# Performance work log

Measured on AMD Instinct MI355X. Metric: run time of the kernel, lower is better.

Reference implementation:

```python
import jax, jax.numpy as jnp
import numpy as np

B, S, HIDDEN = 2, 2048, 2048
HQ, HKV, D = 16, 4, 128
EPS = 1e-6
SCALE = D ** -0.5


def _deinterleave(x):
    # [..., D] interleaved pairs -> [x0,x2,...,x1,x3,...] (half layout)
    *lead, d = x.shape
    return x.reshape(*lead, d // 2, 2).swapaxes(-1, -2).reshape(*lead, d)


def _interleave(x):
    # inverse of _deinterleave
    *lead, d = x.shape
    return x.reshape(*lead, 2, d // 2).swapaxes(-1, -2).reshape(*lead, d)


def _rotate_half(x):
    x1, x2 = jnp.split(x, 2, axis=-1)
    return jnp.concatenate([-x2, x1], axis=-1)


def _rmsnorm(x, w):
    var = jnp.mean(jnp.square(x), axis=-1, keepdims=True)
    return x * jax.lax.rsqrt(var + EPS) * w


def setup_inputs() -> dict:
    key = jax.random.key(0)
    k0, k1, k2, k3, k4 = jax.random.split(key, 5)
    hidden_states = jax.random.normal(k0, (B, S, HIDDEN), jnp.float32)
    cos = jax.random.uniform(k1, (S, D), jnp.float32, -1.0, 1.0)
    sin = jax.random.uniform(k2, (S, D), jnp.float32, -1.0, 1.0)
    qkv_w = jax.random.normal(k3, ((HQ + 2 * HKV) * D, HIDDEN), jnp.float32) * 0.02
    qk_norm_w = jnp.ones((D,), jnp.float32)
    o_w = jax.random.normal(k4, (HIDDEN, HQ * D), jnp.float32) * 0.02
    return {"hidden_states": hidden_states, "cos": cos, "sin": sin,
            "qkv_w": qkv_w, "qk_norm_w": qk_norm_w, "o_w": o_w}


def reference(hidden_states, cos, sin, qkv_w, qk_norm_w, o_w):
    b, s, _ = hidden_states.shape
    qkv = jnp.einsum('bsh,oh->bso', hidden_states, qkv_w)  # [B,S,(HQ+2HKV)*D]
    q = qkv[..., : HQ * D].reshape(b, s, HQ, D)
    k = qkv[..., HQ * D:(HQ + HKV) * D].reshape(b, s, HKV, D)
    v = qkv[..., (HQ + HKV) * D:].reshape(b, s, HKV, D)

    # interleaved-layout RoPE: deinterleave -> rotate-half RoPE -> re-interleave
    q, k = _deinterleave(q), _deinterleave(k)
    cs = cos[None, :, None, :]
    sn = sin[None, :, None, :]
    q = q * cs + _rotate_half(q) * sn
    k = k * cs + _rotate_half(k) * sn
    q, k = _interleave(q), _interleave(k)

    # QK RMSNorm (shared weight over head_dim)
    q = _rmsnorm(q, qk_norm_w)
    k = _rmsnorm(k, qk_norm_w)

    # causal GQA attention
    g = HQ // HKV
    qg = q.reshape(b, s, HKV, g, D)
    scores = jnp.einsum('bshgd,bthd->bhgst', qg, k) * SCALE  # [B,HKV,g,S,S]
    causal = jnp.tril(jnp.ones((s, s), bool))
    scores = jnp.where(causal, scores, jnp.finfo(scores.dtype).min)
    probs = jax.nn.softmax(scores, axis=-1)
    attn = jnp.einsum('bhgst,bthd->bshgd', probs, v).reshape(b, s, HQ * D)

    return jnp.einsum('bsd,od->bso', attn, o_w)
```

## Files before the change

### kernel.cpp

```cpp
#include <hip/hip_runtime.h>
#include <hip/hip_bf16.h>

typedef __bf16 bf16_t;
typedef bf16_t bf16x8 __attribute__((ext_vector_type(8)));
typedef float f32x4 __attribute__((ext_vector_type(4)));
typedef float f32x16 __attribute__((ext_vector_type(16)));
typedef unsigned short u16;
typedef unsigned int u32;

#define B_    2
#define S_    2048
#define HID   2048
#define NQKV  3072
#define HQ_   16
#define HKV_  4
#define D_    128
#define QSCALE_ 0.12751879526600565f

__device__ __forceinline__ u16 f2b(float f) {
    __hip_bfloat16 h = __float2bfloat16(f);
    return *reinterpret_cast<u16*>(&h);
}

__global__ __launch_bounds__(256) void cvt_f32_bf16(const float* __restrict__ in,
                                                    u16* __restrict__ out, int n4) {
    int i = blockIdx.x * 256 + threadIdx.x;
    if (i >= n4) return;
    float4 v = reinterpret_cast<const float4*>(in)[i];
    ushort4 o;
    o.x = f2b(v.x); o.y = f2b(v.y); o.z = f2b(v.z); o.w = f2b(v.w);
    reinterpret_cast<ushort4*>(out)[i] = o;
}

__global__ __launch_bounds__(512, 1) void gemm256_bt(const u16* __restrict__ A,
                                                     const u16* __restrict__ Bm,
                                                     float* __restrict__ C,
                                                     int M, int N, int K) {
    extern __shared__ __align__(16) char smem[];
    u16* Asm = (u16*)smem;
    u16* Bsm = (u16*)smem + 32768;

    const int tid  = threadIdx.x;
    const int lane = tid & 63;
    const int wid  = tid >> 6;
    const int wr = wid >> 2, wc = wid & 3;
    const int lrow = lane & 15, lgrp = lane >> 4;
    const int swz  = (lrow & 7) << 4;
    const int m0 = blockIdx.x * 256, n0 = blockIdx.y * 256;

    const int stRow = tid >> 3;
    const int stCol = ((((tid & 7) * 16) ^ ((stRow & 7) << 4)) >> 1);

    const u16* aBase = A  + (size_t)(m0 + stRow) * K + stCol;
    const u16* bBase = Bm + (size_t)(n0 + stRow) * K + stCol;

    auto glds = [&](const u16* g, u16* l) {
        __builtin_amdgcn_global_load_lds(
            (const __attribute__((address_space(1))) void*)g,
            (__attribute__((address_space(3))) void*)l, 16, 0, 0);
    };
    auto stageA = [&](int buf, int h, int k0) {
        const u16* g = aBase + (size_t)(128 * h) * K + k0;
        u16* d = Asm + buf * 16384 + (1024 * h + tid) * 8;
        glds(g, d);
        glds(g + (size_t)64 * K, d + 512 * 8);
    };
    auto stageB = [&](int buf, int h, int k0) {
        const u16* g = bBase + (size_t)(128 * h) * K + k0;
        u16* d = Bsm + buf * 16384 + (1024 * h + tid) * 8;
        glds(g, d);
        glds(g + (size_t)64 * K, d + 512 * 8);
    };

    f32x4 acc[8][4] = {};
    const int KT = K >> 6;

    stageA(0, 0, 0); stageA(0, 1, 0); stageB(0, 0, 0); stageB(0, 1, 0);
    asm volatile("s_waitcnt vmcnt(0)" ::: "memory");
    __builtin_amdgcn_s_barrier();

    for (int x = 0; x < KT; ++x) {
        const int cur = x & 1;
        const int kn  = (x + 1) << 6;
        const bool pf = (x + 1 < KT);
        const char* aT = (const char*)(Asm + cur * 16384);
        const char* bT = (const char*)(Bsm + cur * 16384);

        auto ldA = [&](int mi, int ks) -> bf16x8 {
            int row = wr * 128 + mi * 16 + lrow;
            return *(const bf16x8*)(aT + row * 128 + ((ks * 64 + lgrp * 16) ^ swz));
        };
        auto ldB = [&](int ni, int ks) -> bf16x8 {
            int row = wc * 64 + ni * 16 + lrow;
            return *(const bf16x8*)(bT + row * 128 + ((ks * 64 + lgrp * 16) ^ swz));
        };

        bf16x8 a[4][2], b[2][2], b2[2][2];

        #pragma unroll
        for (int mi = 0; mi < 4; ++mi) { a[mi][0] = ldA(mi, 0); a[mi][1] = ldA(mi, 1); }
        #pragma unroll
        for (int ni = 0; ni < 2; ++ni) { b[ni][0] = ldB(ni, 0); b[ni][1] = ldB(ni, 1); }
        if (pf) stageA(cur ^ 1, 0, kn);
        __builtin_amdgcn_s_barrier();
        __builtin_amdgcn_s_setprio(1);
        #pragma unroll
        for (int mi = 0; mi < 4; ++mi)
            #pragma unroll
            for (int ni = 0; ni < 2; ++ni) {
                acc[mi][ni] = __builtin_amdgcn_mfma_f32_16x16x32_bf16(a[mi][0], b[ni][0], acc[mi][ni], 0, 0, 0);
                acc[mi][ni] = __builtin_amdgcn_mfma_f32_16x16x32_bf16(a[mi][1], b[ni][1], acc[mi][ni], 0, 0, 0);
            }
        __builtin_amdgcn_s_setprio(0);
        __builtin_amdgcn_s_barrier();

        #pragma unroll
        for (int ni = 0; ni < 2; ++ni) { b2[ni][0] = ldB(ni + 2, 0); b2[ni][1] = ldB(ni + 2, 1); }
        if (pf) stageA(cur ^ 1, 1, kn);
        __builtin_amdgcn_s_barrier();
        __builtin_amdgcn_s_setprio(1);
        #pragma unroll
        for (int mi = 0; mi < 4; ++mi)
            #pragma unroll
            for (int ni = 0; ni < 2; ++ni) {
                acc[mi][ni + 2] = __builtin_amdgcn_mfma_f32_16x16x32_bf16(a[mi][0], b2[ni][0], acc[mi][ni + 2], 0, 0, 0);
                acc[mi][ni + 2] = __builtin_amdgcn_mfma_f32_16x16x32_bf16(a[mi][1], b2[ni][1], acc[mi][ni + 2], 0, 0, 0);
            }
        __builtin_amdgcn_s_setprio(0);
        __builtin_amdgcn_s_barrier();

        #pragma unroll
        for (int mi = 0; mi < 4; ++mi) { a[mi][0] = ldA(mi + 4, 0); a[mi][1] = ldA(mi + 4, 1); }
        if (pf) stageB(cur ^ 1, 0, kn);
        __builtin_amdgcn_s_barrier();
        __builtin_amdgcn_s_setprio(1);
        #pragma unroll
        for (int mi = 0; mi < 4; ++mi)
            #pragma unroll
            for (int ni = 0; ni < 2; ++ni) {
                acc[mi + 4][ni + 2] = __builtin_amdgcn_mfma_f32_16x16x32_bf16(a[mi][0], b2[ni][0], acc[mi + 4][ni + 2], 0, 0, 0);
                acc[mi + 4][ni + 2] = __builtin_amdgcn_mfma_f32_16x16x32_bf16(a[mi][1], b2[ni][1], acc[mi + 4][ni + 2], 0, 0, 0);
            }
        __builtin_amdgcn_s_setprio(0);
        __builtin_amdgcn_s_barrier();

        #pragma unroll
        for (int ni = 0; ni < 2; ++ni) { b[ni][0] = ldB(ni, 0); b[ni][1] = ldB(ni, 1); }
        if (pf) stageB(cur ^ 1, 1, kn);
        __builtin_amdgcn_s_barrier();
        __builtin_amdgcn_s_setprio(1);
        #pragma unroll
        for (int mi = 0; mi < 4; ++mi)
            #pragma unroll
            for (int ni = 0; ni < 2; ++ni) {
                acc[mi + 4][ni] = __builtin_amdgcn_mfma_f32_16x16x32_bf16(a[mi][0], b[ni][0], acc[mi + 4][ni], 0, 0, 0);
                acc[mi + 4][ni] = __builtin_amdgcn_mfma_f32_16x16x32_bf16(a[mi][1], b[ni][1], acc[mi + 4][ni], 0, 0, 0);
            }
        __builtin_amdgcn_s_setprio(0);
        asm volatile("s_waitcnt vmcnt(0)" ::: "memory");
        __builtin_amdgcn_s_barrier();
    }

    #pragma unroll
    for (int mi = 0; mi < 8; ++mi)
        #pragma unroll
        for (int ni = 0; ni < 4; ++ni) {
            int r = m0 + wr * 128 + mi * 16 + lgrp * 4;
            int c = n0 + wc * 64 + ni * 16 + lrow;
            float* p = C + (size_t)r * N + c;
            #pragma unroll
            for (int i = 0; i < 4; ++i) p[(size_t)i * N] = acc[mi][ni][i];
        }
}

__global__ __launch_bounds__(256) void rope_norm_split(const float* __restrict__ qkv,
                                                       const float* __restrict__ cosb,
                                                       const float* __restrict__ sinb,
                                                       const float* __restrict__ nw,
                                                       u16* __restrict__ qb,
                                                       u16* __restrict__ kb,
                                                       u16* __restrict__ vb) {
    const int row  = blockIdx.x;
    const int b    = row >> 11;
    const int s    = row & 2047;
    const int wave = threadIdx.x >> 6;
    const int lane = threadIdx.x & 63;
    const float* base = qkv + (size_t)row * NQKV;

    const float c0 = cosb[s * 128 + lane];
    const float c1 = cosb[s * 128 + 64 + lane];
    const float s0 = sinb[s * 128 + lane];
    const float s1 = sinb[s * 128 + 64 + lane];
    const float w0 = nw[2 * lane];
    const float w1 = nw[2 * lane + 1];

    for (int h = wave; h < HQ_ + HKV_; h += 4) {
        float2 x = *(const float2*)(base + h * 128 + 2 * lane);
        float y0 = x.x * c0 - x.y * s0;
        float y1 = x.y * c1 + x.x * s1;
        float ss = y0 * y0 + y1 * y1;
        #pragma unroll
        for (int off = 32; off; off >>= 1) ss += __shfl_xor(ss, off);
        float r = rsqrtf(ss * (1.0f / 128.0f) + 1e-6f);
        float o0 = y0 * r * w0, o1 = y1 * r * w1;
        if (h < HQ_) {
            u32 pack = (u32)f2b(o0 * QSCALE_) | ((u32)f2b(o1 * QSCALE_) << 16);
            *(u32*)(qb + ((size_t)(b * HQ_ + h) * S_ + s) * D_ + 2 * lane) = pack;
        } else {
            u32 pack = (u32)f2b(o0) | ((u32)f2b(o1) << 16);
            *(u32*)(kb + ((size_t)(b * HKV_ + (h - HQ_)) * S_ + s) * D_ + 2 * lane) = pack;
        }
    }
    {
        int h = wave;
        float2 x = *(const float2*)(base + (HQ_ + HKV_) * 128 + h * 128 + 2 * lane);
        u32 pack = (u32)f2b(x.x) | ((u32)f2b(x.y) << 16);
        *(u32*)(vb + ((size_t)(b * HKV_ + h) * S_ + s) * D_ + 2 * lane) = pack;
    }
}

__global__ __launch_bounds__(256) void transpose_v(const u16* __restrict__ vb,
                                                   u16* __restrict__ vtb) {
    __shared__ u16 t[64][72];
    const int s0 = blockIdx.x * 64, d0 = blockIdx.y * 64, bh = blockIdx.z;
    const u16* src = vb  + (size_t)bh * S_ * D_;
    u16*       dst = vtb + (size_t)bh * D_ * S_;
    const int tid = threadIdx.x;

    {
        int r = tid >> 3, c8 = (tid & 7) * 8;
        #pragma unroll
        for (int p = 0; p < 2; p++) {
            int rr = r + p * 32;
            *(uint4*)&t[rr][c8] = *(const uint4*)(src + (size_t)(s0 + rr) * D_ + d0 + c8);
        }
    }
    __syncthreads();
    {
        int dd = tid & 63;
        int sb = (tid >> 6) * 8;
        #pragma unroll
        for (int p = 0; p < 2; p++) {
            int ss8 = sb + p * 32;
            union { u16 u[8]; uint4 v; } pk;
            #pragma unroll
            for (int j = 0; j < 8; j++) pk.u[j] = t[ss8 + j][dd];
            *(uint4*)(dst + (size_t)(d0 + dd) * S_ + s0 + ss8) = pk.v;
        }
    }
}

__global__ __launch_bounds__(256, 2) void attn_fwd3(const u16* __restrict__ qb,
                                                    const u16* __restrict__ kb,
                                                    const u16* __restrict__ vtb,
                                                    u16* __restrict__ attn) {
    __shared__ __align__(16) u16 Ks[2][64 * 128];
    __shared__ __align__(16) u16 Vs[2][128 * 64];

    const int bh  = blockIdx.y;
    const int qt  = (bh < 16) ? (15 - (int)blockIdx.x) : (int)blockIdx.x;
    const int b   = bh >> 4, hq = bh & 15, hkv = hq >> 2;
    const int tid = threadIdx.x;
    const int wave = tid >> 6, lane = tid & 63;
    const int l31 = lane & 31, hi = lane >> 5;
    const int swz = (l31 & 7) << 4;

    const u16* Q  = qb  + (size_t)(b * HQ_  + hq ) * S_ * D_;
    const u16* Kp = kb  + (size_t)(b * HKV_ + hkv) * S_ * D_;
    const u16* Vt = vtb + (size_t)(b * HKV_ + hkv) * D_ * S_;
    const int q0w = qt * 128 + wave * 32;
    const int qg  = q0w + l31;

    int kSrc[4], vSrc[4], cLds[4];
    #pragma unroll
    for (int p = 0; p < 4; p++) {
        int c = tid + p * 256;
        int kr = c >> 4, kc = ((c & 15) * 16) ^ ((kr & 7) << 4);
        kSrc[p] = kr * D_ + (kc >> 1);
        int vr = c >> 3, vc = ((c & 7) * 16) ^ ((vr & 7) << 4);
        vSrc[p] = vr * S_ + (vc >> 1);
        cLds[p] = c * 16;
    }

    auto STAGE = [&](int buf, int kv0s) {
        const u16* kbase = Kp + (size_t)kv0s * D_;
        const u16* vbase = Vt + kv0s;
        #pragma unroll
        for (int p = 0; p < 4; p++)
            __builtin_amdgcn_global_load_lds(
                (const __attribute__((address_space(1))) void*)(kbase + kSrc[p]),
                (__attribute__((address_space(3))) void*)((char*)Ks[buf] + cLds[p]), 16, 0, 0);
        #pragma unroll
        for (int p = 0; p < 4; p++)
            __builtin_amdgcn_global_load_lds(
                (const __attribute__((address_space(1))) void*)(vbase + vSrc[p]),
                (__attribute__((address_space(3))) void*)((char*)Vs[buf] + cLds[p]), 16, 0, 0);
    };

    bf16x8 qf[8];
    #pragma unroll
    for (int ds = 0; ds < 8; ds++)
        qf[ds] = *(const bf16x8*)(Q + (size_t)qg * D_ + ds * 16 + hi * 8);

    float m_run = -1e30f, l_run = 0.f;
    f32x16 oacc[4] = {};

    const int nkt = 2 * qt + 2;
    STAGE(0, 0);

    for (int kt = 0; kt < nkt; kt++) {
        const int cur = kt & 1;
        const int kv0 = kt * 64;
        if (kt + 1 < nkt) {
            STAGE(cur ^ 1, kv0 + 64);
            asm volatile("s_waitcnt vmcnt(8)" ::: "memory");
        } else {
            asm volatile("s_waitcnt vmcnt(0)" ::: "memory");
        }
        __builtin_amdgcn_s_barrier();

        const char* ksb = (const char*)Ks[cur];
        const char* vsb = (const char*)Vs[cur];
        const char* rb0 = ksb + l31 * 256;
        const char* rb1 = rb0 + 32 * 256;
        bf16x8 kA[8], kB[8];
        #pragma unroll
        for (int ds = 0; ds < 8; ds++) kA[ds] = *(const bf16x8*)(rb0 + ((ds * 32 + hi * 16) ^ swz));
        #pragma unroll
        for (int ds = 0; ds < 8; ds++) kB[ds] = *(const bf16x8*)(rb1 + ((ds * 32 + hi * 16) ^ swz));

        f32x16 sc[2] = {};
        __builtin_amdgcn_s_setprio(1);
        #pragma unroll
        for (int ds = 0; ds < 8; ds++)
            sc[0] = __builtin_amdgcn_mfma_f32_32x32x16_bf16(kA[ds], qf[ds], sc[0], 0, 0, 0);
        #pragma unroll
        for (int ds = 0; ds < 8; ds++)
            sc[1] = __builtin_amdgcn_mfma_f32_32x32x16_bf16(kB[ds], qf[ds], sc[1], 0, 0, 0);
        __builtin_amdgcn_s_setprio(0);

        bf16x8 vf[4][4];
        #pragma unroll
        for (int ks = 0; ks < 4; ks++)
            #pragma unroll
            for (int d4 = 0; d4 < 4; d4++)
                vf[ks][d4] = *(const bf16x8*)(vsb + (d4 * 32 + l31) * 128
                                                  + ((ks * 32 + hi * 16) ^ swz));
        __builtin_amdgcn_s_barrier();

        if (kv0 + 63 > q0w) {
            #pragma unroll
            for (int blk = 0; blk < 2; blk++)
                #pragma unroll
                for (int r = 0; r < 16; r++) {
                    int kvg = kv0 + blk * 32 + (r & 3) + 8 * (r >> 2) + 4 * hi;
                    if (kvg > qg) sc[blk][r] = -1e30f;
                }
        }

        float t16[16];
        #pragma unroll
        for (int r = 0; r < 16; r++) t16[r] = fmaxf(sc[0][r], sc[1][r]);
        #pragma unroll
        for (int r = 0; r < 8; r++) t16[r] = fmaxf(t16[r], t16[r + 8]);
        #pragma unroll
        for (int r = 0; r < 4; r++) t16[r] = fmaxf(t16[r], t16[r + 4]);
        float mt = fmaxf(fmaxf(t16[0], t16[1]), fmaxf(t16[2], t16[3]));
        mt = fmaxf(mt, __shfl_xor(mt, 32));

        bool noDefer = !__all(mt <= m_run + 8.0f);
        float mnew = m_run;
        if (noDefer) {
            mnew = fmaxf(m_run, mt);
            float alpha = __builtin_amdgcn_exp2f(m_run - mnew);
            l_run *= alpha;
            #pragma unroll
            for (int d4 = 0; d4 < 4; d4++)
                #pragma unroll
                for (int r = 0; r < 16; r++) oacc[d4][r] *= alpha;
            m_run = mnew;
        }

        float la = 0.f;
        u32 pk0[8], pk1[8];
        #pragma unroll
        for (int g = 0; g < 4; g++)
            #pragma unroll
            for (int e = 0; e < 2; e++) {
                float a0 = __builtin_amdgcn_exp2f(sc[0][g * 4 + 2 * e]     - mnew);
                float b0 = __builtin_amdgcn_exp2f(sc[0][g * 4 + 2 * e + 1] - mnew);
                float a1 = __builtin_amdgcn_exp2f(sc[1][g * 4 + 2 * e]     - mnew);
                float b1 = __builtin_amdgcn_exp2f(sc[1][g * 4 + 2 * e + 1] - mnew);
                la += (a0 + b0) + (a1 + b1);
                pk0[g * 2 + e] = (u32)f2b(a0) | ((u32)f2b(b0) << 16);
                pk1[g * 2 + e] = (u32)f2b(a1) | ((u32)f2b(b1) << 16);
            }
        la += __shfl_xor(la, 32);
        l_run += la;

        u32 qk0[8], qk1[8];
        #pragma unroll
        for (int i = 0; i < 8; i++) {
            qk0[i] = __shfl_xor(pk0[i], 32);
            qk1[i] = __shfl_xor(pk1[i], 32);
        }

        #pragma unroll
        for (int ks = 0; ks < 4; ks++) {
            const int i0 = (ks & 1) * 4;
            union { u32 w[4]; bf16x8 v; } pfv;
            if (ks & 2) {
                pfv.w[0] = hi ? qk1[i0 + 2] : pk1[i0 + 0];
                pfv.w[1] = hi ? qk1[i0 + 3] : pk1[i0 + 1];
                pfv.w[2] = hi ? pk1[i0 + 2] : qk1[i0 + 0];
                pfv.w[3] = hi ? pk1[i0 + 3] : qk1[i0 + 1];
            } else {
                pfv.w[0] = hi ? qk0[i0 + 2] : pk0[i0 + 0];
                pfv.w[1] = hi ? qk0[i0 + 3] : pk0[i0 + 1];
                pfv.w[2] = hi ? pk0[i0 + 2] : qk0[i0 + 0];
                pfv.w[3] = hi ? pk0[i0 + 3] : qk0[i0 + 1];
            }
            __builtin_amdgcn_s_setprio(1);
            #pragma unroll
            for (int d4 = 0; d4 < 4; d4++)
                oacc[d4] = __builtin_amdgcn_mfma_f32_32x32x16_bf16(vf[ks][d4], pfv.v, oacc[d4], 0, 0, 0);
            __builtin_amdgcn_s_setprio(0);
        }
    }

    const float inv = 1.0f / l_run;
    u16* sl = (u16*)Ks + wave * (32 * 128);
    #pragma unroll
    for (int d4 = 0; d4 < 4; d4++)
        #pragma unroll
        for (int rp = 0; rp < 8; rp++) {
            int dbyte = d4 * 64 + 16 * (rp >> 1) + 8 * hi + 4 * (rp & 1);
            u32 w = (u32)f2b(oacc[d4][rp * 2] * inv)
                  | ((u32)f2b(oacc[d4][rp * 2 + 1] * inv) << 16);
            *(u32*)((char*)sl + l31 * 256 + (dbyte ^ swz)) = w;
        }
    #pragma unroll
    for (int j = 0; j < 8; j++) {
        int c = lane + j * 64;
        int qL = c >> 4, dc = c & 15;
        uint4 v = *(uint4*)((char*)sl + qL * 256 + ((dc * 16) ^ ((qL & 7) << 4)));
        int qrow = qt * 128 + wave * 32 + qL;
        *(uint4*)(attn + (size_t)(b * S_ + qrow) * (HQ_ * D_) + hq * D_ + dc * 8) = v;
    }
}

extern "C" void kernel_launch(void* const* d_in, const int* in_sizes, int n_in,
                              void* d_out, int out_size, void* d_ws, size_t ws_size,
                              hipStream_t stream) {
    const float* hidden = (const float*)d_in[0];
    const float* cosb   = (const float*)d_in[1];
    const float* sinb   = (const float*)d_in[2];
    const float* qkvw   = (const float*)d_in[3];
    const float* nw     = (const float*)d_in[4];
    const float* ow     = (const float*)d_in[5];
    float* out = (float*)d_out;

    const size_t M  = (size_t)B_ * S_;
    char* ws = (char*)d_ws;
    size_t off = 0;
    u16*   hb    = (u16*)(ws + off); off += M * HID * 2;
    u16*   wqkvb = (u16*)(ws + off); off += (size_t)NQKV * HID * 2;
    u16*   wob   = (u16*)(ws + off); off += (size_t)HID * (HQ_ * D_) * 2;
    float* qkv   = (float*)(ws + off); off += M * NQKV * 4;
    u16*   qb2   = (u16*)(ws + off); off += (size_t)B_ * HQ_  * S_ * D_ * 2;
    u16*   kb2   = (u16*)(ws + off); off += (size_t)B_ * HKV_ * S_ * D_ * 2;
    u16*   vb2   = (u16*)(ws + off); off += (size_t)B_ * HKV_ * S_ * D_ * 2;
    u16*   vtb   = (u16*)(ws + off); off += (size_t)B_ * HKV_ * S_ * D_ * 2;
    u16*   attn  = hb;

    {
        int n4 = (int)(M * HID / 4);
        cvt_f32_bf16<<<(n4 + 255) / 256, 256, 0, stream>>>(hidden, hb, n4);
    }
    {
        int n4 = NQKV * HID / 4;
        cvt_f32_bf16<<<(n4 + 255) / 256, 256, 0, stream>>>(qkvw, wqkvb, n4);
    }
    {
        int n4 = HID * (HQ_ * D_) / 4;
        cvt_f32_bf16<<<(n4 + 255) / 256, 256, 0, stream>>>(ow, wob, n4);
    }

    const int smemSz = 131072;
    hipFuncSetAttribute(reinterpret_cast<const void*>(gemm256_bt),
                        hipFuncAttributeMaxDynamicSharedMemorySize, smemSz);

    gemm256_bt<<<dim3(M / 256, NQKV / 256), 512, smemSz, stream>>>(hb, wqkvb, qkv,
                                                                   (int)M, NQKV, HID);

    rope_norm_split<<<(int)M, 256, 0, stream>>>(qkv, cosb, sinb, nw, qb2, kb2, vb2);

    transpose_v<<<dim3(S_ / 64, D_ / 64, B_ * HKV_), 256, 0, stream>>>(vb2, vtb);

    attn_fwd3<<<dim3(16, B_ * HQ_), 256, 0, stream>>>(qb2, kb2, vtb, attn);

    gemm256_bt<<<dim3(M / 256, HID / 256), 512, smemSz, stream>>>(attn, wob, out,
                                                                  (int)M, HID, HQ_ * D_);
}
```

Baseline: 234.2 us.

## Shrink GEMM tiles to 128x256, emit bf16 QKV, single-buffer V in attention

The GEMM tile goes from 256x256 to 128x256, which doubles the block count so the CUs are better filled, and adds an XCD-aware block swizzle. The whole next K-tile is now prefetched up front and there are fewer barriers. The QKV GEMM now writes bf16 directly, which halves intermediate traffic, and rope_norm reads bf16. The attention kernel single-buffers V to raise occupancy to 3 blocks and reorders the grid so heads vary fastest. The risks are lower per-block reuse in the GEMM, V loads that are exposed, and slightly lower precision because qkv is rounded before RoPE and norm.

```diff
diff --git a/kernel.cpp b/kernel.cpp
--- a/kernel.cpp
+++ b/kernel.cpp
@@ -21,6 +21,12 @@
     __hip_bfloat16 h = __float2bfloat16(f);
     return *reinterpret_cast<u16*>(&h);
 }
+__device__ __forceinline__ float b2f(u32 u) {
+    u32 v = u << 16;
+    float f;
+    __builtin_memcpy(&f, &v, 4);
+    return f;
+}
 
 __global__ __launch_bounds__(256) void cvt_f32_bf16(const float* __restrict__ in,
                                                     u16* __restrict__ out, int n4) {
@@ -32,13 +38,12 @@
     reinterpret_cast<ushort4*>(out)[i] = o;
 }
 
-__global__ __launch_bounds__(512, 1) void gemm256_bt(const u16* __restrict__ A,
-                                                     const u16* __restrict__ Bm,
-                                                     float* __restrict__ C,
-                                                     int M, int N, int K) {
+template<bool BF16OUT>
+__global__ __launch_bounds__(512, 1) void gemm128x256(const u16* __restrict__ A,
+                                                      const u16* __restrict__ Bm,
+                                                      void* __restrict__ Cv,
+                                                      int M, int N, int K) {
     extern __shared__ __align__(16) char smem[];
-    u16* Asm = (u16*)smem;
-    u16* Bsm = (u16*)smem + 32768;
 
     const int tid  = threadIdx.x;
     const int lane = tid & 63;
@@ -46,11 +51,15 @@
     const int wr = wid >> 2, wc = wid & 3;
     const int lrow = lane & 15, lgrp = lane >> 4;
     const int swz  = (lrow & 7) << 4;
-    const int m0 = blockIdx.x * 256, n0 = blockIdx.y * 256;
+
+    const int gx = gridDim.x;
+    const int nwg = gx * gridDim.y;
+    const int id = blockIdx.x + blockIdx.y * gx;
+    const int swid = (id & 7) * (nwg >> 3) + (id >> 3);
+    const int m0 = (swid % gx) * 128, n0 = (swid / gx) * 256;
 
     const int stRow = tid >> 3;
     const int stCol = ((((tid & 7) * 16) ^ ((stRow & 7) << 4)) >> 1);
-
     const u16* aBase = A  + (size_t)(m0 + stRow) * K + stCol;
     const u16* bBase = Bm + (size_t)(n0 + stRow) * K + stCol;
 
@@ -59,35 +68,34 @@
             (const __attribute__((address_space(1))) void*)g,
             (__attribute__((address_space(3))) void*)l, 16, 0, 0);
     };
-    auto stageA = [&](int buf, int h, int k0) {
-        const u16* g = aBase + (size_t)(128 * h) * K + k0;
-        u16* d = Asm + buf * 16384 + (1024 * h + tid) * 8;
+    auto stA = [&](int buf, int k0) {
+        u16* d = (u16*)(smem + buf * 49152) + tid * 8;
+        glds(aBase + k0, d);
+        glds(aBase + (size_t)64 * K + k0, d + 512 * 8);
+    };
+    auto stB = [&](int buf, int h, int k0) {
+        u16* d = (u16*)(smem + buf * 49152 + 16384 + h * 16384) + tid * 8;
+        const u16* g = bBase + (size_t)(128 * h) * K + k0;
         glds(g, d);
         glds(g + (size_t)64 * K, d + 512 * 8);
     };
-    auto stageB = [&](int buf, int h, int k0) {
-        const u16* g = bBase + (size_t)(128 * h) * K + k0;
-        u16* d = Bsm + buf * 16384 + (1024 * h + tid) * 8;
-        glds(g, d);
-        glds(g + (size_t)64 * K, d + 512 * 8);
-    };
-
-    f32x4 acc[8][4] = {};
+
+    f32x4 acc[4][4] = {};
     const int KT = K >> 6;
 
-    stageA(0, 0, 0); stageA(0, 1, 0); stageB(0, 0, 0); stageB(0, 1, 0);
+    stA(0, 0); stB(0, 0, 0); stB(0, 1, 0);
     asm volatile("s_waitcnt vmcnt(0)" ::: "memory");
     __builtin_amdgcn_s_barrier();
 
-    for (int x = 0; x < KT; ++x) {
-        const int cur = x & 1;
-        const int kn  = (x + 1) << 6;
-        const bool pf = (x + 1 < KT);
-        const char* aT = (const char*)(Asm + cur * 16384);
-        const char* bT = (const char*)(Bsm + cur * 16384);
+    for (int t = 0; t < KT; ++t) {
+        const int cur = t & 1;
+        const int kn  = (t + 1) << 6;
+        const bool pf = (t + 1 < KT);
+        const char* aT = smem + cur * 49152;
+        const char* bT = aT + 16384;
 
         auto ldA = [&](int mi, int ks) -> bf16x8 {
-            int row = wr * 128 + mi * 16 + lrow;
+            int row = wr * 64 + mi * 16 + lrow;
             return *(const bf16x8*)(aT + row * 128 + ((ks * 64 + lgrp * 16) ^ swz));
         };
         auto ldB = [&](int ni, int ks) -> bf16x8 {
@@ -101,7 +109,7 @@
         for (int mi = 0; mi < 4; ++mi) { a[mi][0] = ldA(mi, 0); a[mi][1] = ldA(mi, 1); }
         #pragma unroll
         for (int ni = 0; ni < 2; ++ni) { b[ni][0] = ldB(ni, 0); b[ni][1] = ldB(ni, 1); }
-        if (pf) stageA(cur ^ 1, 0, kn);
+        if (pf) { stA(cur ^ 1, kn); stB(cur ^ 1, 0, kn); stB(cur ^ 1, 1, kn); }
         __builtin_amdgcn_s_barrier();
         __builtin_amdgcn_s_setprio(1);
         #pragma unroll
@@ -112,11 +120,9 @@
                 acc[mi][ni] = __builtin_amdgcn_mfma_f32_16x16x32_bf16(a[mi][1], b[ni][1], acc[mi][ni], 0, 0, 0);
             }
         __builtin_amdgcn_s_setprio(0);
-        __builtin_amdgcn_s_barrier();
 
         #pragma unroll
         for (int ni = 0; ni < 2; ++ni) { b2[ni][0] = ldB(ni + 2, 0); b2[ni][1] = ldB(ni + 2, 1); }
-        if (pf) stageA(cur ^ 1, 1, kn);
         __builtin_amdgcn_s_barrier();
         __builtin_amdgcn_s_setprio(1);
         #pragma unroll
@@ -127,53 +133,31 @@
                 acc[mi][ni + 2] = __builtin_amdgcn_mfma_f32_16x16x32_bf16(a[mi][1], b2[ni][1], acc[mi][ni + 2], 0, 0, 0);
             }
         __builtin_amdgcn_s_setprio(0);
-        __builtin_amdgcn_s_barrier();
-
-        #pragma unroll
-        for (int mi = 0; mi < 4; ++mi) { a[mi][0] = ldA(mi + 4, 0); a[mi][1] = ldA(mi + 4, 1); }
-        if (pf) stageB(cur ^ 1, 0, kn);
-        __builtin_amdgcn_s_barrier();
-        __builtin_amdgcn_s_setprio(1);
-        #pragma unroll
-        for (int mi = 0; mi < 4; ++mi)
-            #pragma unroll
-            for (int ni = 0; ni < 2; ++ni) {
-                acc[mi + 4][ni + 2] = __builtin_amdgcn_mfma_f32_16x16x32_bf16(a[mi][0], b2[ni][0], acc[mi + 4][ni + 2], 0, 0, 0);
-                acc[mi + 4][ni + 2] = __builtin_amdgcn_mfma_f32_16x16x32_bf16(a[mi][1], b2[ni][1], acc[mi + 4][ni + 2], 0, 0, 0);
+        if (pf) {
+            asm volatile("s_waitcnt vmcnt(0)" ::: "memory");
+            __builtin_amdgcn_s_barrier();
+        }
+    }
+
+    #pragma unroll
+    for (int mi = 0; mi < 4; ++mi)
+        #pragma unroll
+        for (int ni = 0; ni < 4; ++ni) {
+            int r = m0 + wr * 64 + mi * 16 + lgrp * 4;
+            int c = n0 + wc * 64 + ni * 16 + lrow;
+            if (BF16OUT) {
+                u16* o = (u16*)Cv + (size_t)r * N + c;
+                #pragma unroll
+                for (int i = 0; i < 4; ++i) o[(size_t)i * N] = f2b(acc[mi][ni][i]);
+            } else {
+                float* p = (float*)Cv + (size_t)r * N + c;
+                #pragma unroll
+                for (int i = 0; i < 4; ++i) p[(size_t)i * N] = acc[mi][ni][i];
             }
-        __builtin_amdgcn_s_setprio(0);
-        __builtin_amdgcn_s_barrier();
-
-        #pragma unroll
-        for (int ni = 0; ni < 2; ++ni) { b[ni][0] = ldB(ni, 0); b[ni][1] = ldB(ni, 1); }
-        if (pf) stageB(cur ^ 1, 1, kn);
-        __builtin_amdgcn_s_barrier();
-        __builtin_amdgcn_s_setprio(1);
-        #pragma unroll
-        for (int mi = 0; mi < 4; ++mi)
-            #pragma unroll
-            for (int ni = 0; ni < 2; ++ni) {
-                acc[mi + 4][ni] = __builtin_amdgcn_mfma_f32_16x16x32_bf16(a[mi][0], b[ni][0], acc[mi + 4][ni], 0, 0, 0);
-                acc[mi + 4][ni] = __builtin_amdgcn_mfma_f32_16x16x32_bf16(a[mi][1], b[ni][1], acc[mi + 4][ni], 0, 0, 0);
-            }
-        __builtin_amdgcn_s_setprio(0);
-        asm volatile("s_waitcnt vmcnt(0)" ::: "memory");
-        __builtin_amdgcn_s_barrier();
-    }
-
-    #pragma unroll
-    for (int mi = 0; mi < 8; ++mi)
-        #pragma unroll
-        for (int ni = 0; ni < 4; ++ni) {
-            int r = m0 + wr * 128 + mi * 16 + lgrp * 4;
-            int c = n0 + wc * 64 + ni * 16 + lrow;
-            float* p = C + (size_t)r * N + c;
-            #pragma unroll
-            for (int i = 0; i < 4; ++i) p[(size_t)i * N] = acc[mi][ni][i];
-        }
-}
-
-__global__ __launch_bounds__(256) void rope_norm_split(const float* __restrict__ qkv,
+        }
+}
+
+__global__ __launch_bounds__(256) void rope_norm_split(const u16* __restrict__ qkvb,
                                                        const float* __restrict__ cosb,
                                                        const float* __restrict__ sinb,
                                                        const float* __restrict__ nw,
@@ -185,7 +169,7 @@
     const int s    = row & 2047;
     const int wave = threadIdx.x >> 6;
     const int lane = threadIdx.x & 63;
-    const float* base = qkv + (size_t)row * NQKV;
+    const u16* base = qkvb + (size_t)row * NQKV;
 
     const float c0 = cosb[s * 128 + lane];
     const float c1 = cosb[s * 128 + 64 + lane];
@@ -195,9 +179,10 @@
     const float w1 = nw[2 * lane + 1];
 
     for (int h = wave; h < HQ_ + HKV_; h += 4) {
-        float2 x = *(const float2*)(base + h * 128 + 2 * lane);
-        float y0 = x.x * c0 - x.y * s0;
-        float y1 = x.y * c1 + x.x * s1;
+        u32 xw = *(const u32*)(base + h * 128 + 2 * lane);
+        float x0 = b2f(xw & 0xffffu), x1 = b2f(xw >> 16);
+        float y0 = x0 * c0 - x1 * s0;
+        float y1 = x1 * c1 + x0 * s1;
         float ss = y0 * y0 + y1 * y1;
         #pragma unroll
         for (int off = 32; off; off >>= 1) ss += __shfl_xor(ss, off);
@@ -213,9 +198,8 @@
     }
     {
         int h = wave;
-        float2 x = *(const float2*)(base + (HQ_ + HKV_) * 128 + h * 128 + 2 * lane);
-        u32 pack = (u32)f2b(x.x) | ((u32)f2b(x.y) << 16);
-        *(u32*)(vb + ((size_t)(b * HKV_ + h) * S_ + s) * D_ + 2 * lane) = pack;
+        u32 xw = *(const u32*)(base + (HQ_ + HKV_) * 128 + h * 128 + 2 * lane);
+        *(u32*)(vb + ((size_t)(b * HKV_ + h) * S_ + s) * D_ + 2 * lane) = xw;
     }
 }
 
@@ -250,15 +234,15 @@
     }
 }
 
-__global__ __launch_bounds__(256, 2) void attn_fwd3(const u16* __restrict__ qb,
+__global__ __launch_bounds__(256, 3) void attn_fwd5(const u16* __restrict__ qb,
                                                     const u16* __restrict__ kb,
                                                     const u16* __restrict__ vtb,
                                                     u16* __restrict__ attn) {
     __shared__ __align__(16) u16 Ks[2][64 * 128];
-    __shared__ __align__(16) u16 Vs[2][128 * 64];
-
-    const int bh  = blockIdx.y;
-    const int qt  = (bh < 16) ? (15 - (int)blockIdx.x) : (int)blockIdx.x;
+    __shared__ __align__(16) u16 Vs[128 * 64];
+
+    const int bh  = blockIdx.x;
+    const int qt  = 15 - (int)blockIdx.y;
     const int b   = bh >> 4, hq = bh & 15, hkv = hq >> 2;
     const int tid = threadIdx.x;
     const int wave = tid >> 6, lane = tid & 63;
@@ -282,19 +266,21 @@
         cLds[p] = c * 16;
     }
 
-    auto STAGE = [&](int buf, int kv0s) {
+    auto STAGE_K = [&](int buf, int kv0s) {
         const u16* kbase = Kp + (size_t)kv0s * D_;
-        const u16* vbase = Vt + kv0s;
         #pragma unroll
         for (int p = 0; p < 4; p++)
             __builtin_amdgcn_global_load_lds(
                 (const __attribute__((address_space(1))) void*)(kbase + kSrc[p]),
                 (__attribute__((address_space(3))) void*)((char*)Ks[buf] + cLds[p]), 16, 0, 0);
+    };
+    auto STAGE_V = [&](int kv0s) {
+        const u16* vbase = Vt + kv0s;
         #pragma unroll
         for (int p = 0; p < 4; p++)
             __builtin_amdgcn_global_load_lds(
                 (const __attribute__((address_space(1))) void*)(vbase + vSrc[p]),
-                (__attribute__((address_space(3))) void*)((char*)Vs[buf] + cLds[p]), 16, 0, 0);
+                (__attribute__((address_space(3))) void*)((char*)Vs + cLds[p]), 16, 0, 0);
     };
 
     bf16x8 qf[8];
@@ -306,21 +292,21 @@
     f32x16 oacc[4] = {};
 
     const int nkt = 2 * qt + 2;
-    STAGE(0, 0);
+    STAGE_K(0, 0);
+    STAGE_V(0);
 
     for (int kt = 0; kt < nkt; kt++) {
         const int cur = kt & 1;
         const int kv0 = kt * 64;
         if (kt + 1 < nkt) {
-            STAGE(cur ^ 1, kv0 + 64);
-            asm volatile("s_waitcnt vmcnt(8)" ::: "memory");
+            STAGE_K(cur ^ 1, kv0 + 64);
+            asm volatile("s_waitcnt vmcnt(4)" ::: "memory");
         } else {
             asm volatile("s_waitcnt vmcnt(0)" ::: "memory");
         }
         __builtin_amdgcn_s_barrier();
 
         const char* ksb = (const char*)Ks[cur];
-        const char* vsb = (const char*)Vs[cur];
         const char* rb0 = ksb + l31 * 256;
         const char* rb1 = rb0 + 32 * 256;
         bf16x8 kA[8], kB[8];
@@ -339,6 +325,7 @@
             sc[1] = __builtin_amdgcn_mfma_f32_32x32x16_bf16(kB[ds], qf[ds], sc[1], 0, 0, 0);
         __builtin_amdgcn_s_setprio(0);
 
+        const char* vsb = (const char*)Vs;
         bf16x8 vf[4][4];
         #pragma unroll
         for (int ks = 0; ks < 4; ks++)
@@ -346,7 +333,10 @@
             for (int d4 = 0; d4 < 4; d4++)
                 vf[ks][d4] = *(const bf16x8*)(vsb + (d4 * 32 + l31) * 128
                                                   + ((ks * 32 + hi * 16) ^ swz));
+        asm volatile("s_waitcnt lgkmcnt(0)" ::: "memory");
+        __builtin_amdgcn_sched_barrier(0);
         __builtin_amdgcn_s_barrier();
+        if (kt + 1 < nkt) STAGE_V(kv0 + 64);
 
         if (kv0 + 63 > q0w) {
             #pragma unroll
@@ -466,7 +456,7 @@
     u16*   hb    = (u16*)(ws + off); off += M * HID * 2;
     u16*   wqkvb = (u16*)(ws + off); off += (size_t)NQKV * HID * 2;
     u16*   wob   = (u16*)(ws + off); off += (size_t)HID * (HQ_ * D_) * 2;
-    float* qkv   = (float*)(ws + off); off += M * NQKV * 4;
+    u16*   qkvb  = (u16*)(ws + off); off += M * NQKV * 2;
     u16*   qb2   = (u16*)(ws + off); off += (size_t)B_ * HQ_  * S_ * D_ * 2;
     u16*   kb2   = (u16*)(ws + off); off += (size_t)B_ * HKV_ * S_ * D_ * 2;
     u16*   vb2   = (u16*)(ws + off); off += (size_t)B_ * HKV_ * S_ * D_ * 2;
@@ -486,19 +476,23 @@
         cvt_f32_bf16<<<(n4 + 255) / 256, 256, 0, stream>>>(ow, wob, n4);
     }
 
-    const int smemSz = 131072;
-    hipFuncSetAttribute(reinterpret_cast<const void*>(gemm256_bt),
+    const int smemSz = 98304;
+    auto* g1 = gemm128x256<true>;
+    auto* g2 = gemm128x256<false>;
+    hipFuncSetAttribute(reinterpret_cast<const void*>(g1),
                         hipFuncAttributeMaxDynamicSharedMemorySize, smemSz);
-
-    gemm256_bt<<<dim3(M / 256, NQKV / 256), 512, smemSz, stream>>>(hb, wqkvb, qkv,
-                                                                   (int)M, NQKV, HID);
-
-    rope_norm_split<<<(int)M, 256, 0, stream>>>(qkv, cosb, sinb, nw, qb2, kb2, vb2);
+    hipFuncSetAttribute(reinterpret_cast<const void*>(g2),
+                        hipFuncAttributeMaxDynamicSharedMemorySize, smemSz);
+
+    gemm128x256<true><<<dim3(M / 128, NQKV / 256), 512, smemSz, stream>>>(
+        hb, wqkvb, qkvb, (int)M, NQKV, HID);
+
+    rope_norm_split<<<(int)M, 256, 0, stream>>>(qkvb, cosb, sinb, nw, qb2, kb2, vb2);
 
     transpose_v<<<dim3(S_ / 64, D_ / 64, B_ * HKV_), 256, 0, stream>>>(vb2, vtb);
 
-    attn_fwd3<<<dim3(16, B_ * HQ_), 256, 0, stream>>>(qb2, kb2, vtb, attn);
-
-    gemm256_bt<<<dim3(M / 256, HID / 256), 512, smemSz, stream>>>(attn, wob, out,
-                                                                  (int)M, HID, HQ_ * D_);
-}
+    attn_fwd5<<<dim3(B_ * HQ_, 16), 256, 0, stream>>>(qb2, kb2, vtb, attn);
+
+    gemm128x256<false><<<dim3(M / 128, HID / 256), 512, smemSz, stream>>>(
+        attn, wob, out, (int)M, HID, HQ_ * D_);
+}
```

After: 426.3 us. 1.82x slower.
